# Kernel tuning notes

Hardware: AMD Instinct MI355X
Metric: run time of the kernel (lower is better)

## Reference

```python
import jax, jax.numpy as jnp
import numpy as np

BATCH, SEQ, CHANNELS, KSIZE = 4, 4096, 2048, 4


def setup_inputs() -> dict:
    key = jax.random.key(0)
    kx, kw = jax.random.split(key)
    x = jax.random.normal(kx, (BATCH, SEQ, CHANNELS), dtype=jnp.float32)
    # flax param init: normal(stddev=0.02), shape (kernel_size, channels)
    kernel = jax.random.normal(kw, (KSIZE, CHANNELS), dtype=jnp.float32) * 0.02
    return {"x": x, "kernel": kernel}


def reference(x, kernel):
    # Causal depthwise short conv: y[:, t] = silu(sum_j kernel[j] * x[:, t - j])
    # (the scan's window * kernel[::-1] unrolls to exactly this), with zero
    # left-padding of K-1 steps standing in for cache=None -> zeros.
    B, T, C = x.shape
    K = kernel.shape[0]
    kf = kernel.astype(x.dtype)
    cache = jnp.zeros((B, K - 1, C), dtype=x.dtype)
    xp = jnp.concatenate([cache, x], axis=1)  # [B, T+K-1, C]
    # Small fixed loop over kernel taps (K=4), fully parallel over time.
    y = kf[0][None, None, :] * xp[:, K - 1 : K - 1 + T, :]
    for j in range(1, K):
        y = y + kf[j][None, None, :] * xp[:, K - 1 - j : K - 1 - j + T, :]
    y = jax.nn.silu(y)
    # next_cache after the scan = last K-1 inputs of the padded stream
    next_cache = xp[:, T:, :]  # [B, K-1, C]
    return y, next_cache
```

## Files before the change

### kernel.cpp

```cpp
#include <hip/hip_runtime.h>
#include <math.h>


#define B_   4
#define T_   4096
#define C_   2048
#define K_   4
#define C4_  (C_ / 4)
#define TG_  4
#define NT_  (T_ / TG_)

__device__ __forceinline__ float silu_f(float v) {
    return v * __builtin_amdgcn_rcpf(1.f + __expf(-v));
}

__global__ __launch_bounds__(256, 4) void dwconv_silu_kernel(
    const float4* __restrict__ x,
    const float4* __restrict__ kern,
    float4* __restrict__ y,
    float4* __restrict__ cache)
{
    const int j  = blockIdx.x * 256 + threadIdx.x;
    const int c4 = j & (C4_ - 1);
    const int tg = (j >> 9) & (NT_ - 1);
    const int b  = j >> 19;
    const int t0 = tg * TG_;

    const float4* xp = x + (((size_t)b * T_ + t0) * C4_ + c4);

    const float4 k0 = kern[0 * C4_ + c4];
    const float4 k1 = kern[1 * C4_ + c4];
    const float4 k2 = kern[2 * C4_ + c4];
    const float4 k3 = kern[3 * C4_ + c4];

    float4 m3, m2, m1;
    if (t0 == 0) {
        m3 = m2 = m1 = make_float4(0.f, 0.f, 0.f, 0.f);
    } else {
        m3 = xp[-3 * C4_];
        m2 = xp[-2 * C4_];
        m1 = xp[-1 * C4_];
    }
    const float4 a0 = xp[0 * C4_];
    const float4 a1 = xp[1 * C4_];
    const float4 a2 = xp[2 * C4_];
    const float4 a3 = xp[3 * C4_];

    __builtin_amdgcn_sched_barrier(0);

#define CONV1(r, a, w1, w2, w3)                                              \
    r.x = fmaf(k0.x, a.x, fmaf(k1.x, w1.x, fmaf(k2.x, w2.x, k3.x * w3.x)));  \
    r.y = fmaf(k0.y, a.y, fmaf(k1.y, w1.y, fmaf(k2.y, w2.y, k3.y * w3.y)));  \
    r.z = fmaf(k0.z, a.z, fmaf(k1.z, w1.z, fmaf(k2.z, w2.z, k3.z * w3.z)));  \
    r.w = fmaf(k0.w, a.w, fmaf(k1.w, w1.w, fmaf(k2.w, w2.w, k3.w * w3.w)));  \
    r.x = silu_f(r.x); r.y = silu_f(r.y); r.z = silu_f(r.z); r.w = silu_f(r.w);

    float4 r0, r1, r2, r3;
    CONV1(r0, a0, m1, m2, m3)
    CONV1(r1, a1, a0, m1, m2)
    CONV1(r2, a2, a1, a0, m1)
    CONV1(r3, a3, a2, a1, a0)
#undef CONV1

    float4* yp = y + (((size_t)b * T_ + t0) * C4_ + c4);
    yp[0 * C4_] = r0;
    yp[1 * C4_] = r1;
    yp[2 * C4_] = r2;
    yp[3 * C4_] = r3;

    if (tg == NT_ - 1) {
        float4* cb = cache + (size_t)b * (K_ - 1) * C4_ + c4;
        cb[0 * C4_] = a1;
        cb[1 * C4_] = a2;
        cb[2 * C4_] = a3;
    }
}

extern "C" void kernel_launch(void* const* d_in, const int* in_sizes, int n_in,
                              void* d_out, int out_size, void* d_ws, size_t ws_size,
                              hipStream_t stream)
{
    const float4* x    = (const float4*)d_in[0];
    const float4* kern = (const float4*)d_in[1];
    float*        out  = (float*)d_out;

    float4* y     = (float4*)out;
    float4* cache = (float4*)(out + (size_t)B_ * T_ * C_);

    const int total_threads = B_ * NT_ * C4_;
    dim3 grid(total_threads / 256);
    dim3 block(256);
    dwconv_silu_kernel<<<grid, block, 0, stream>>>(x, kern, y, cache);
}
```

Measured before the change: 227.7 us.

## Process eight timesteps per thread and remap workgroups across XCDs

Each thread now covers eight consecutive timesteps instead of four, so the three-step halo reload is spread over more outputs and redundant reads of x drop. Workgroup IDs are also remapped so consecutive logical blocks land on the same XCD, which is meant to improve L2 locality for the overlapping halo rows. Stores are interleaved with compute to limit register pressure. The trade-off is half as many threads and more live registers per thread, which may reduce occupancy.

```diff
diff --git a/kernel.cpp b/kernel.cpp
--- a/kernel.cpp
+++ b/kernel.cpp
@@ -7,8 +7,9 @@
 #define C_   2048
 #define K_   4
 #define C4_  (C_ / 4)
-#define TG_  4
+#define TG_  8
 #define NT_  (T_ / TG_)
+#define NXCD_ 8
 
 __device__ __forceinline__ float silu_f(float v) {
     return v * __builtin_amdgcn_rcpf(1.f + __expf(-v));
@@ -20,10 +21,14 @@
     float4* __restrict__ y,
     float4* __restrict__ cache)
 {
-    const int j  = blockIdx.x * 256 + threadIdx.x;
+    const int nwg   = (B_ * NT_ * C4_) / 256;
+    const int chunk = nwg / NXCD_;
+    const int wg    = (blockIdx.x % NXCD_) * chunk + blockIdx.x / NXCD_;
+
+    const int j  = wg * 256 + threadIdx.x;
     const int c4 = j & (C4_ - 1);
     const int tg = (j >> 9) & (NT_ - 1);
-    const int b  = j >> 19;
+    const int b  = j >> 18;
     const int t0 = tg * TG_;
 
     const float4* xp = x + (((size_t)b * T_ + t0) * C4_ + c4);
@@ -45,6 +50,10 @@
     const float4 a1 = xp[1 * C4_];
     const float4 a2 = xp[2 * C4_];
     const float4 a3 = xp[3 * C4_];
+    const float4 a4 = xp[4 * C4_];
+    const float4 a5 = xp[5 * C4_];
+    const float4 a6 = xp[6 * C4_];
+    const float4 a7 = xp[7 * C4_];
 
     __builtin_amdgcn_sched_barrier(0);
 
@@ -55,24 +64,23 @@
     r.w = fmaf(k0.w, a.w, fmaf(k1.w, w1.w, fmaf(k2.w, w2.w, k3.w * w3.w)));  \
     r.x = silu_f(r.x); r.y = silu_f(r.y); r.z = silu_f(r.z); r.w = silu_f(r.w);
 
-    float4 r0, r1, r2, r3;
-    CONV1(r0, a0, m1, m2, m3)
-    CONV1(r1, a1, a0, m1, m2)
-    CONV1(r2, a2, a1, a0, m1)
-    CONV1(r3, a3, a2, a1, a0)
+    float4* yp = y + (((size_t)b * T_ + t0) * C4_ + c4);
+    float4 r;
+    CONV1(r, a0, m1, m2, m3)  yp[0 * C4_] = r;
+    CONV1(r, a1, a0, m1, m2)  yp[1 * C4_] = r;
+    CONV1(r, a2, a1, a0, m1)  yp[2 * C4_] = r;
+    CONV1(r, a3, a2, a1, a0)  yp[3 * C4_] = r;
+    CONV1(r, a4, a3, a2, a1)  yp[4 * C4_] = r;
+    CONV1(r, a5, a4, a3, a2)  yp[5 * C4_] = r;
+    CONV1(r, a6, a5, a4, a3)  yp[6 * C4_] = r;
+    CONV1(r, a7, a6, a5, a4)  yp[7 * C4_] = r;
 #undef CONV1
-
-    float4* yp = y + (((size_t)b * T_ + t0) * C4_ + c4);
-    yp[0 * C4_] = r0;
-    yp[1 * C4_] = r1;
-    yp[2 * C4_] = r2;
-    yp[3 * C4_] = r3;
 
     if (tg == NT_ - 1) {
         float4* cb = cache + (size_t)b * (K_ - 1) * C4_ + c4;
-        cb[0 * C4_] = a1;
-        cb[1 * C4_] = a2;
-        cb[2 * C4_] = a3;
+        cb[0 * C4_] = a5;
+        cb[1 * C4_] = a6;
+        cb[2 * C4_] = a7;
     }
 }
 
```

New measurement: 239.0 us. +5.0%, slower.
